# Kernel optimization log

Hardware: AMD Instinct MI355X
Metric: run time of the kernel (lower is better)

The kernel has to match this reference:

```python
import jax, jax.numpy as jnp
import numpy as np

B, N, D = 8, 4096, 256
T = 768          # text_dim
E = 4            # num_experts
K = 2            # top_k
GS = 64          # grid_size = img_size // patch_size
WS = 8           # swin window size
NH = 4           # swin heads
MODES = 16       # fno modes
HID = 4 * D      # mlp hidden


def setup_inputs() -> dict:
    key = jax.random.key(0)
    ks = jax.random.split(key, 40)
    rn = lambda k, s, sc=0.02: jax.random.normal(k, s, jnp.float32) * sc
    return {
        "x": jax.random.normal(ks[0], (B, N, D), jnp.float32),
        "text_embedding": jax.random.normal(ks[1], (B, T), jnp.float32),
        # TopKGating: Linear(D+T->D), ReLU, Linear(D->E)
        "g1_w": rn(ks[2], (D, D + T)), "g1_b": jnp.zeros((D,), jnp.float32),
        "g2_w": rn(ks[3], (E, D)), "g2_b": jnp.zeros((E,), jnp.float32),
        # FNOExpert: SpectralConv2d complex weights (real/imag) + 1x1 conv
        "fno_w1r": rn(ks[4], (D, D, MODES, MODES), 1.0 / D), "fno_w1i": rn(ks[5], (D, D, MODES, MODES), 1.0 / D),
        "fno_w2r": rn(ks[6], (D, D, MODES, MODES), 1.0 / D), "fno_w2i": rn(ks[7], (D, D, MODES, MODES), 1.0 / D),
        "fno_cw": rn(ks[8], (D, D)), "fno_cb": jnp.zeros((D,), jnp.float32),
        # MLPExpert #1
        "m1_w1": rn(ks[9], (HID, D)), "m1_b1": jnp.zeros((HID,), jnp.float32),
        "m1_w2": rn(ks[10], (D, HID)), "m1_b2": jnp.zeros((D,), jnp.float32),
        # WindowAttentionExpert
        "a_ln1w": jnp.ones((D,), jnp.float32), "a_ln1b": jnp.zeros((D,), jnp.float32),
        "a_qkvw": rn(ks[11], (3 * D, D)), "a_qkvb": jnp.zeros((3 * D,), jnp.float32),
        "a_ow": rn(ks[12], (D, D)), "a_ob": jnp.zeros((D,), jnp.float32),
        "a_ln2w": jnp.ones((D,), jnp.float32), "a_ln2b": jnp.zeros((D,), jnp.float32),
        "a_mw1": rn(ks[13], (HID, D)), "a_mb1": jnp.zeros((HID,), jnp.float32),
        "a_mw2": rn(ks[14], (D, HID)), "a_mb2": jnp.zeros((D,), jnp.float32),
        # MLPExpert #2 (extra expert to reach num_experts=4)
        "m2_w1": rn(ks[15], (HID, D)), "m2_b1": jnp.zeros((HID,), jnp.float32),
        "m2_w2": rn(ks[16], (D, HID)), "m2_b2": jnp.zeros((D,), jnp.float32),
    }


def _gelu(v):
    return jax.nn.gelu(v, approximate=False)


def _ln(v, g, b, eps=1e-5):
    m = v.mean(-1, keepdims=True)
    var = ((v - m) ** 2).mean(-1, keepdims=True)
    return (v - m) * jax.lax.rsqrt(var + eps) * g + b


def reference(x, text_embedding, g1_w, g1_b, g2_w, g2_b,
              fno_w1r, fno_w1i, fno_w2r, fno_w2i, fno_cw, fno_cb,
              m1_w1, m1_b1, m1_w2, m1_b2,
              a_ln1w, a_ln1b, a_qkvw, a_qkvb, a_ow, a_ob,
              a_ln2w, a_ln2b, a_mw1, a_mb1, a_mw2, a_mb2,
              m2_w1, m2_b1, m2_w2, m2_b2):
    Bb, Nn, Dd = x.shape

    # ---- TopKGating ----
    feat = jnp.concatenate([x.mean(axis=1), text_embedding], axis=1)   # [B, D+T]
    h = jax.nn.relu(feat @ g1_w.T + g1_b)
    logits = h @ g2_w.T + g2_b                                         # [B, E]
    vals, idx = jax.lax.top_k(logits, K)
    w = jax.nn.softmax(vals, axis=1)                                   # [B, K]
    # per-(sample, expert) combine weight; indices are constants
    combine = (w[..., None] * jax.nn.one_hot(idx, E, dtype=x.dtype)).sum(axis=1)  # [B, E]

    # ---- Expert 0: FNO ----
    def fno(v):
        xg = v.transpose(0, 2, 1).reshape(Bb, Dd, GS, GS)              # [B, D, H, W]
        xft = jnp.fft.rfft2(xg)                                        # [B, D, H, W//2+1]
        w1 = fno_w1r + 1j * fno_w1i
        w2 = fno_w2r + 1j * fno_w2i
        lo = jnp.einsum('bixy,ioxy->boxy', xft[:, :, :MODES, :MODES], w1)
        hi = jnp.einsum('bixy,ioxy->boxy', xft[:, :, -MODES:, :MODES], w2)
        out_ft = jnp.zeros_like(xft)
        out_ft = out_ft.at[:, :, :MODES, :MODES].set(lo)
        out_ft = out_ft.at[:, :, -MODES:, :MODES].set(hi)
        x1 = jnp.fft.irfft2(out_ft, s=(GS, GS))
        x2 = jnp.einsum('bihw,oi->bohw', xg, fno_cw) + fno_cb[None, :, None, None]
        out = _gelu(x1 + x2)
        return out.reshape(Bb, Dd, Nn).transpose(0, 2, 1) + v

    # ---- MLP experts ----
    def mlp(v, w1, b1, w2, b2):
        return _gelu(v @ w1.T + b1) @ w2.T + b2 + v

    # ---- Expert 2: window attention ----
    def win_attn(v):
        xs = _ln(v, a_ln1w, a_ln1b).reshape(Bb, GS, GS, Dd)
        nw = GS // WS
        xw = xs.reshape(Bb, nw, WS, nw, WS, Dd).transpose(0, 1, 3, 2, 4, 5)
        xw = xw.reshape(-1, WS * WS, Dd)                               # [B*nw*nw, L, D]
        qkv = xw @ a_qkvw.T + a_qkvb
        q, k, vv = jnp.split(qkv, 3, axis=-1)
        dh = Dd // NH
        heads = lambda t: t.reshape(-1, WS * WS, NH, dh).transpose(0, 2, 1, 3)
        q, k, vv = heads(q), heads(k), heads(vv)
        attn = jax.nn.softmax(q @ k.transpose(0, 1, 3, 2) / jnp.sqrt(jnp.float32(dh)), axis=-1)
        o = (attn @ vv).transpose(0, 2, 1, 3).reshape(-1, WS * WS, Dd) @ a_ow.T + a_ob
        o = o.reshape(Bb, nw, nw, WS, WS, Dd).transpose(0, 1, 3, 2, 4, 5).reshape(Bb, Nn, Dd)
        v2 = v + o
        return v2 + (_gelu(_ln(v2, a_ln2w, a_ln2b) @ a_mw1.T + a_mb1) @ a_mw2.T + a_mb2)

    outs = [fno(x),
            mlp(x, m1_w1, m1_b1, m1_w2, m1_b2),
            win_attn(x),
            mlp(x, m2_w1, m2_b1, m2_w2, m2_b2)]
    final = sum(combine[:, e, None, None] * outs[e] for e in range(E))
    return final, w
```

## Files before the change

kernel.cpp:

```cpp
#include <hip/hip_runtime.h>
#include <math.h>

#define BB 8
#define NN 4096
#define DDIM 256
#define TT 768
#define BND (BB*NN*DDIM)

typedef unsigned short ushort_t;
typedef short bf16x8 __attribute__((ext_vector_type(8)));
typedef float f32x4 __attribute__((ext_vector_type(4)));

__device__ __forceinline__ float gelu_f(float v){
    float y = 0.7978845608028654f * v * (1.0f + 0.044715f * v * v);
    float ay = fabsf(y);
    float e = __expf(-2.0f * ay);
    float th = 1.0f - 2.0f * e / (1.0f + e);
    th = copysignf(th, y);
    return 0.5f * v * (1.0f + th);
}
__device__ __forceinline__ ushort_t f2bf(float f){
    union { float f; unsigned int u; } v; v.f = f;
    unsigned int u = v.u;
    u += 0x7FFFu + ((u >> 16) & 1u);
    return (ushort_t)(u >> 16);
}
__device__ __forceinline__ float bf2f(ushort_t h){
    union { unsigned int u; float f; } v; v.u = ((unsigned int)h) << 16;
    return v.f;
}
__device__ __forceinline__ float pk_re(unsigned int p){
    union { unsigned int u; float f; } v; v.u = p << 16; return v.f;
}
__device__ __forceinline__ float pk_im(unsigned int p){
    union { unsigned int u; float f; } v; v.u = p & 0xffff0000u; return v.f;
}
#define GLOAD16(gp, lp) __builtin_amdgcn_global_load_lds( \
    (__attribute__((address_space(1))) const void*)(gp),  \
    (__attribute__((address_space(3))) void*)(lp), 16, 0, 0)

__global__ __launch_bounds__(256) void k_xcvt2(const float4* __restrict__ x,
    const float* __restrict__ lng, const float* __restrict__ lnb,
    ushort_t* __restrict__ xbf, ushort_t* __restrict__ xlnbf, float4* __restrict__ outp,
    float* __restrict__ partialA){
    int w = threadIdx.x >> 6, lane = threadIdx.x & 63;
    int row = blockIdx.x*4 + w;
    size_t i4 = (size_t)row*64 + lane;
    float4 v = x[i4];
    outp[i4] = v;
    float vv[4] = {v.x, v.y, v.z, v.w};
    __shared__ float sda[4][256];
    *(float4*)&sda[w][lane*4] = v;
    float s = (vv[0]+vv[1])+(vv[2]+vv[3]);
    float s2 = (vv[0]*vv[0]+vv[1]*vv[1])+(vv[2]*vv[2]+vv[3]*vv[3]);
    for (int off=32; off; off>>=1){ s += __shfl_down(s, off); s2 += __shfl_down(s2, off); }
    float m = __shfl(s, 0) * (1.0f/DDIM);
    float var = __shfl(s2, 0) * (1.0f/DDIM) - m*m;
    float r = rsqrtf(var + 1e-5f);
    int c0 = lane*4;
    #pragma unroll
    for (int u=0;u<4;++u){
        size_t i = i4*4 + u;
        xbf[i] = f2bf(vv[u]);
        xlnbf[i] = f2bf((vv[u]-m)*r*lng[c0+u] + lnb[c0+u]);
    }
    __syncthreads();
    if (w==0){
        float4 a = *(const float4*)&sda[0][lane*4];
        float4 b4 = *(const float4*)&sda[1][lane*4];
        float4 c4 = *(const float4*)&sda[2][lane*4];
        float4 d4 = *(const float4*)&sda[3][lane*4];
        float4 sum = make_float4(a.x+b4.x+c4.x+d4.x, a.y+b4.y+c4.y+d4.y,
                                 a.z+b4.z+c4.z+d4.z, a.w+b4.w+c4.w+d4.w);
        *(float4*)&partialA[(size_t)blockIdx.x*256 + lane*4] = sum;
    }
}

__global__ __launch_bounds__(256) void k_meanB(const float* __restrict__ partialA, float* __restrict__ partialB){
    int seg = blockIdx.x, b = blockIdx.y, t = threadIdx.x;
    const float* p = partialA + ((size_t)(b*1024 + seg*64))*256 + t;
    float s0=0,s1=0,s2=0,s3=0;
    #pragma unroll
    for (int c=0;c<64;c+=4){
        s0 += p[(size_t)c*256];
        s1 += p[(size_t)(c+1)*256];
        s2 += p[(size_t)(c+2)*256];
        s3 += p[(size_t)(c+3)*256];
    }
    partialB[((size_t)b*16 + seg)*256 + t] = (s0+s1)+(s2+s3);
}

__global__ __launch_bounds__(256) void k_gate1(const float* __restrict__ partial, const float* __restrict__ text,
    const float* __restrict__ g1w, const float* __restrict__ g1b, float* __restrict__ hs){
    int d = blockIdx.x, t = threadIdx.x;
    int w = t >> 6, lane = t & 63;
    float xm[BB];
    #pragma unroll
    for (int b=0;b<BB;++b){
        float s = 0.f;
        #pragma unroll
        for (int c=0;c<16;++c) s += partial[((size_t)b*16 + c)*256 + t];
        xm[b] = s * (1.0f/NN);
    }
    const float* wrow = g1w + (size_t)d*(DDIM+TT);
    float w0 = wrow[t], w1 = wrow[256+t], w2 = wrow[512+t], w3 = wrow[768+t];
    float acc[BB];
    #pragma unroll
    for (int b=0;b<BB;++b){
        const float* tx = text + (size_t)b*TT;
        acc[b] = xm[b]*w0 + tx[t]*w1 + tx[256+t]*w2 + tx[512+t]*w3;
    }
    #pragma unroll
    for (int b=0;b<BB;++b)
        for (int off=32; off; off>>=1) acc[b] += __shfl_down(acc[b], off);
    __shared__ float red[BB][4];
    if (lane==0)
        #pragma unroll
        for (int b=0;b<BB;++b) red[b][w] = acc[b];
    __syncthreads();
    if (t < BB){
        float s = red[t][0]+red[t][1]+red[t][2]+red[t][3] + g1b[d];
        hs[t*DDIM + d] = fmaxf(s, 0.0f);
    }
}

__global__ __launch_bounds__(64) void k_gate2(const float* __restrict__ hs,
    const float* __restrict__ g2w, const float* __restrict__ g2b,
    float* __restrict__ combine, float* __restrict__ wout){
    __shared__ float lg[BB][4];
    int t = threadIdx.x;
    if (t < 32){
        int b = t>>2, e = t&3;
        float a = g2b[e];
        const float* w2 = g2w + e*DDIM;
        const float* h = hs + b*DDIM;
        for (int o=0;o<DDIM;o+=4)
            a += h[o]*w2[o] + h[o+1]*w2[o+1] + h[o+2]*w2[o+2] + h[o+3]*w2[o+3];
        lg[b][e] = a;
    }
    __syncthreads();
    if (t < BB){
        int b = t;
        int i1=0; float v1=lg[b][0];
        for (int e=1;e<4;++e){ if (lg[b][e] > v1){ v1=lg[b][e]; i1=e; } }
        int i2=0; float v2=-3.0e38f; bool found=false;
        for (int e=0;e<4;++e){ if (e==i1) continue; if (!found || lg[b][e] > v2){ v2=lg[b][e]; i2=e; found=true; } }
        float e2 = expf(v2 - v1);
        float inv = 1.0f/(1.0f + e2);
        float w0 = inv, w1 = e2*inv;
        float cv[4] = {0.f,0.f,0.f,0.f};
        cv[i1] = w0; cv[i2] = w1;
        for (int e=0;e<4;++e) combine[b*4+e] = cv[e];
        wout[b*2+0] = w0; wout[b*2+1] = w1;
    }
}

__global__ __launch_bounds__(256) void k_cvtw(
    const float* __restrict__ s0, const float* __restrict__ s1, const float* __restrict__ s2,
    const float* __restrict__ s3, const float* __restrict__ s4, const float* __restrict__ s5,
    const float* __restrict__ s6, const float* __restrict__ s7, const float* __restrict__ s8,
    ushort_t* __restrict__ dst){
    const int off[10] = {0,196608,262144,524288,786432,1048576,1310720,1572864,1835008,1900544};
    const float* srcs[9] = {s0,s1,s2,s3,s4,s5,s6,s7,s8};
    int i = (blockIdx.x*256 + threadIdx.x)*8;
    if (i >= 1900544) return;
    int seg = 0;
    #pragma unroll
    for (int k=1;k<9;++k) if (i >= off[k]) seg = k;
    const float* s = srcs[seg] + (i - off[seg]);
    ushort_t* d = dst + i;
    #pragma unroll
    for (int u=0;u<8;++u) d[u] = f2bf(s[u]);
}

__global__ __launch_bounds__(256) void k_v2cvt2(const float4* __restrict__ v2,
    const float* __restrict__ lng, const float* __restrict__ lnb,
    ushort_t* __restrict__ dstbf, const float* __restrict__ combine){
    int w = threadIdx.x >> 6, lane = threadIdx.x & 63;
    int row = blockIdx.x*4 + w;
    if (combine[(row>>12)*4+2]==0.0f) return;
    size_t i4 = (size_t)row*64 + lane;
    float4 v = v2[i4];
    float vv[4] = {v.x, v.y, v.z, v.w};
    float s = (vv[0]+vv[1])+(vv[2]+vv[3]);
    float s2 = (vv[0]*vv[0]+vv[1]*vv[1])+(vv[2]*vv[2]+vv[3]*vv[3]);
    for (int off=32; off; off>>=1){ s += __shfl_down(s, off); s2 += __shfl_down(s2, off); }
    float m = __shfl(s, 0) * (1.0f/DDIM);
    float var = __shfl(s2, 0) * (1.0f/DDIM) - m*m;
    float r = rsqrtf(var + 1e-5f);
    int c0 = lane*4;
    #pragma unroll
    for (int u=0;u<4;++u)
        dstbf[i4*4+u] = f2bf((vv[u]-m)*r*lng[c0+u] + lnb[c0+u]);
}

__global__ __launch_bounds__(256) void k_fft_w2(const ushort_t* __restrict__ xbf, float* __restrict__ F1,
                                                const float* __restrict__ combine){
    int h = blockIdx.x, b = blockIdx.y;
    if (combine[b*4+0]==0.0f) return;
    __shared__ ushort_t img[64*256];
    __shared__ float ct[64], st[64];
    int t = threadIdx.x;
    if (t < 64){ float ang = (float)t * 0.09817477042468103f; ct[t]=cosf(ang); st[t]=sinf(ang); }
    {
        const uint4* src = (const uint4*)(xbf + ((size_t)b*NN + h*64)*DDIM);
        uint4* dst4 = (uint4*)img;
        for (int i=t; i<2048; i+=256) dst4[i] = src[i];
    }
    __syncthreads();
    float re[16], im[16];
    #pragma unroll
    for (int ky=0;ky<16;++ky){ re[ky]=0.f; im[ky]=0.f; }
    for (int w=0; w<64; ++w){
        float v = bf2f(img[w*256 + t]);
        #pragma unroll
        for (int ky=0; ky<16; ++ky){
            int m = (ky*w)&63;
            re[ky] += v*ct[m];
            im[ky] -= v*st[m];
        }
    }
    float2* o = (float2*)(F1 + (((size_t)(b*DDIM + t))*1024 + h*16)*2);
    #pragma unroll
    for (int ky=0;ky<16;++ky) o[ky] = make_float2(re[ky], im[ky]);
}

__global__ __launch_bounds__(256) void k_fft_h(const float* __restrict__ F1,
                                               unsigned int* __restrict__ F2pk,
                                               const float* __restrict__ combine){
    int bd = blockIdx.x; int b = bd>>8;
    if (combine[b*4+0]==0.0f) return;
    __shared__ float f1[2048];
    __shared__ float ct[64], st[64];
    int t = threadIdx.x;
    if (t < 64){ float ang = (float)t * 0.09817477042468103f; ct[t]=cosf(ang); st[t]=sinf(ang); }
    const float* src = F1 + (size_t)bd*2048;
    for (int i=t;i<2048;i+=256) f1[i]=src[i];
    __syncthreads();
    for (int task=t; task<512; task+=256){
        int c = task>>8, kxp = (task>>4)&15, ky = task&15;
        int kx = c ? 48+kxp : kxp;
        float re=0.f, im=0.f;
        #pragma unroll
        for (int h=0;h<64;++h){
            int m = (kx*h)&63;
            float ar = f1[(h*16+ky)*2], ai = f1[(h*16+ky)*2+1];
            re += ar*ct[m] + ai*st[m];
            im += ai*ct[m] - ar*st[m];
        }
        F2pk[(size_t)bd*512 + task] = (((unsigned int)f2bf(im)) << 16) | (unsigned int)f2bf(re);
    }
}

__global__ __launch_bounds__(256, 8) void k_specmul12(const unsigned int* __restrict__ F2pk,
    const float* __restrict__ w1r, const float* __restrict__ w1i,
    const float* __restrict__ w2r, const float* __restrict__ w2i,
    float* __restrict__ Gp, const float* __restrict__ combine){
    bool any=false;
    for (int b=0;b<BB;++b) any = any || (combine[b*4]!=0.0f);
    if (!any) return;
    int t  = threadIdx.x;
    int o0 = blockIdx.x * 2;
    int c  = blockIdx.y;
    int s  = blockIdx.z;
    const float* Wr0 = (c ? w2r : w1r) + ((size_t)(s*32)*DDIM + o0)*256 + t;
    const float* Wi0 = (c ? w2i : w1i) + ((size_t)(s*32)*DDIM + o0)*256 + t;
    const unsigned int* Fp = F2pk + (size_t)(s*32)*512 + c*256 + t;
    float ar[2][BB], ai[2][BB];
    #pragma unroll
    for (int oo=0;oo<2;++oo)
        #pragma unroll
        for (int b=0;b<BB;++b){ ar[oo][b]=0.f; ai[oo][b]=0.f; }
    for (int ii=0; ii<32; ++ii){
        float wr0 = __builtin_nontemporal_load(Wr0);
        float wr1 = __builtin_nontemporal_load(Wr0 + 256);
        float wi0 = __builtin_nontemporal_load(Wi0);
        float wi1 = __builtin_nontemporal_load(Wi0 + 256);
        unsigned int f[BB];
        #pragma unroll
        for (int b=0;b<BB;++b)
            f[b] = Fp[(size_t)b*131072];
        Wr0 += 65536; Wi0 += 65536; Fp += 512;
        #pragma unroll
        for (int b=0;b<BB;++b){
            float fr = pk_re(f[b]);
            float fi = pk_im(f[b]);
            ar[0][b] += fr*wr0 - fi*wi0;
            ai[0][b] += fr*wi0 + fi*wr0;
            ar[1][b] += fr*wr1 - fi*wi1;
            ai[1][b] += fr*wi1 + fi*wr1;
        }
    }
    #pragma unroll
    for (int oo=0;oo<2;++oo)
        for (int b=0;b<BB;++b){
            float* g = Gp + ((((size_t)s*BB + b)*DDIM + o0+oo)*512 + c*256 + t)*2;
            __builtin_nontemporal_store(ar[oo][b], g);
            __builtin_nontemporal_store(ai[oo][b], g+1);
        }
}

__global__ __launch_bounds__(256) void k_ifft_h(const float* __restrict__ Gp, float* __restrict__ Z,
                                                const float* __restrict__ combine){
    int bd = blockIdx.x; int b = bd>>8;
    if (combine[b*4+0]==0.0f) return;
    __shared__ float g[1024];
    __shared__ float ct[64], st[64];
    int t=threadIdx.x;
    if (t < 64){ float ang = (float)t * 0.09817477042468103f; ct[t]=cosf(ang); st[t]=sinf(ang); }
    {
        f32x4 v = (f32x4){0.f,0.f,0.f,0.f};
        #pragma unroll
        for (int s=0;s<8;++s){
            const f32x4* p = (const f32x4*)(Gp + (size_t)s*2097152 + (size_t)bd*1024);
            v += __builtin_nontemporal_load(p + t);
        }
        *(f32x4*)(g + t*4) = v;
    }
    __syncthreads();
    for (int task=t;task<1024;task+=256){
        int h=task>>4, ky=task&15;
        float re=0.f, im=0.f;
        #pragma unroll
        for (int c=0;c<2;++c){
            #pragma unroll
            for (int kxp=0;kxp<16;++kxp){
                int kx = c ? 48+kxp : kxp;
                int m = (kx*h)&63;
                int gi = (c*256 + kxp*16 + ky)*2;
                float gr=g[gi], gim=g[gi+1];
                re += gr*ct[m] - gim*st[m];
                im += gr*st[m] + gim*ct[m];
            }
        }
        float2* o = (float2*)(Z + ((size_t)bd*1024 + task)*2);
        *o = make_float2(re*(1.0f/64.0f), im*(1.0f/64.0f));
    }
}

__global__ __launch_bounds__(256) void k_fno_out(const float* __restrict__ Z, const ushort_t* __restrict__ X2,
    const float* __restrict__ combine, float* __restrict__ out){
    int h = blockIdx.x, b = blockIdx.y;
    float cb = combine[b*4];
    if (cb==0.0f) return;
    __shared__ float ct[64], st[64];
    int t = threadIdx.x;
    if (t < 64){ float ang = (float)t * 0.09817477042468103f; ct[t]=cosf(ang); st[t]=sinf(ang); }
    __syncthreads();
    float zr[16], zi[16];
    const float* zp = Z + (((size_t)(b*DDIM + t)*64 + h)*16)*2;
    #pragma unroll
    for (int ky=0;ky<16;++ky){
        float2 v = *(const float2*)(zp + ky*2);
        zr[ky]=v.x; zi[ky]=v.y;
    }
    for (int w=0;w<64;++w){
        float s = zr[0];
        #pragma unroll
        for (int ky=1;ky<16;++ky){
            int m = (ky*w)&63;
            s += 2.0f*(zr[ky]*ct[m] - zi[ky]*st[m]);
        }
        s *= (1.0f/64.0f);
        size_t idx = ((size_t)b*NN + h*64 + w)*DDIM + t;
        out[idx] += cb * gelu_f(s + bf2f(X2[idx]));
    }
}

template<int EPI>
__global__ __launch_bounds__(256) void k_bgemm(
    const ushort_t* __restrict__ A, const ushort_t* __restrict__ W, const float* __restrict__ bias,
    void* __restrict__ dst, const float* __restrict__ combine, int expert, int K, int N,
    const float* __restrict__ xres, float* __restrict__ out)
{
    int tiles_n = N >> 7;
    int tm = blockIdx.x / tiles_n, tn = blockIdx.x - tm*tiles_n;
    int row0 = tm << 7, col0 = tn << 7;
    float scale = combine[(row0>>12)*4 + expert];
    if (scale == 0.0f) return;
    __shared__ __align__(16) ushort_t As[8192];
    __shared__ __align__(16) ushort_t Bs[8192];
    int t = threadIdx.x;
    int w = t >> 6, lane = t & 63;
    int wr = w >> 1, wc = w & 1;
    int lrow = lane >> 3, lk8 = (lane & 7) * 8;
    f32x4 acc[4][4];
    #pragma unroll
    for (int m=0;m<4;++m)
        #pragma unroll
        for (int n=0;n<4;++n) acc[m][n] = (f32x4){0.f,0.f,0.f,0.f};
    int afr = lane & 15, akr = (lane >> 4) * 8;
    for (int k0=0; k0<K; k0+=64){
        #pragma unroll
        for (int it=0; it<4; ++it){
            int c = it*4 + w;
            const ushort_t* ga = A + (size_t)(row0 + c*8 + lrow)*K + k0 + lk8;
            GLOAD16(ga, As + c*512);
            const ushort_t* gb = W + (size_t)(col0 + c*8 + lrow)*K + k0 + lk8;
            GLOAD16(gb, Bs + c*512);
        }
        __syncthreads();
        #pragma unroll
        for (int kk=0; kk<2; ++kk){
            bf16x8 af[4], bfr[4];
            #pragma unroll
            for (int m=0;m<4;++m)
                af[m] = *(const bf16x8*)(As + (wr*64 + m*16 + afr)*64 + kk*32 + akr);
            #pragma unroll
            for (int n=0;n<4;++n)
                bfr[n] = *(const bf16x8*)(Bs + (wc*64 + n*16 + afr)*64 + kk*32 + akr);
            #pragma unroll
            for (int m=0;m<4;++m)
                #pragma unroll
                for (int n=0;n<4;++n)
                    acc[m][n] = __builtin_amdgcn_mfma_f32_16x16x32_bf16(af[m], bfr[n], acc[m][n], 0, 0, 0);
        }
        __syncthreads();
    }
    int rbase = row0 + wr*64 + (lane>>4)*4;
    int cbase = col0 + wc*64 + (lane&15);
    #pragma unroll
    for (int n=0;n<4;++n){
        int col = cbase + n*16;
        float bcol = bias[col];
        #pragma unroll
        for (int m=0;m<4;++m){
            int r0 = rbase + m*16;
            f32x4 a = acc[m][n];
            #pragma unroll
            for (int j=0;j<4;++j){
                int r = r0 + j;
                float v = a[j] + bcol;
                if (EPI==0)      ((ushort_t*)dst)[(size_t)r*N + col] = f2bf(v);
                else if (EPI==1) ((ushort_t*)dst)[(size_t)r*N + col] = f2bf(gelu_f(v));
                else if (EPI==2) out[(size_t)r*DDIM + col] += scale * v;
                else if (EPI==3){
                    ((float*)dst)[(size_t)r*DDIM + col] = xres[(size_t)r*DDIM + col] + v;
                    out[(size_t)r*DDIM + col] += scale * v;
                }
            }
        }
    }
}

__global__ __launch_bounds__(256) void k_attn(const ushort_t* __restrict__ QKV, ushort_t* __restrict__ O,
                                              const float* __restrict__ combine){
    int wh = blockIdx.x;
    int w = wh>>2, head = wh&3;
    int b = w>>6;
    if (combine[b*4+2]==0.0f) return;
    int i1 = (w>>3)&7, i2 = w&7;
    __shared__ float A1[64][64];
    __shared__ float kk[64][65];
    __shared__ float S[64][65];
    int t = threadIdx.x;
    for (int idx=t; idx<4096; idx+=256){
        int l = idx>>6, dc = idx&63;
        int n = b*NN + (i1*8 + (l>>3))*64 + i2*8 + (l&7);
        const ushort_t* qrow = QKV + (size_t)n*768;
        A1[l][dc] = bf2f(qrow[head*64+dc]);
        kk[l][dc] = bf2f(qrow[256+head*64+dc]);
    }
    __syncthreads();
    for (int idx=t; idx<4096; idx+=256){
        int i=idx>>6, j=idx&63;
        float s=0.f;
        #pragma unroll 8
        for (int dc=0;dc<64;++dc) s += A1[i][dc]*kk[j][dc];
        S[i][j] = s * 0.125f;
    }
    __syncthreads();
    for (int idx=t; idx<4096; idx+=256){
        int l = idx>>6, dc = idx&63;
        int n = b*NN + (i1*8 + (l>>3))*64 + i2*8 + (l&7);
        A1[l][dc] = bf2f(QKV[(size_t)n*768 + 512 + head*64 + dc]);
    }
    __syncthreads();
    if (t < 64){
        float mx = -3.0e38f;
        for (int j=0;j<64;++j) mx = fmaxf(mx, S[t][j]);
        float sum=0.f;
        for (int j=0;j<64;++j){ float e = expf(S[t][j]-mx); S[t][j]=e; sum+=e; }
        float inv = 1.0f/sum;
        for (int j=0;j<64;++j) S[t][j] *= inv;
    }
    __syncthreads();
    for (int idx=t; idx<4096; idx+=256){
        int i=idx>>6, dc=idx&63;
        float s=0.f;
        #pragma unroll 8
        for (int j=0;j<64;++j) s += S[i][j]*A1[j][dc];
        int n = b*NN + (i1*8 + (i>>3))*64 + i2*8 + (i&7);
        O[(size_t)n*DDIM + head*64 + dc] = f2bf(s);
    }
}

extern "C" void kernel_launch(void* const* d_in, const int* in_sizes, int n_in,
                              void* d_out, int out_size, void* d_ws, size_t ws_size,
                              hipStream_t stream) {
    (void)in_sizes; (void)n_in; (void)out_size; (void)ws_size;
    const float* x      = (const float*)d_in[0];
    const float* text   = (const float*)d_in[1];
    const float* g1_w   = (const float*)d_in[2];
    const float* g1_b   = (const float*)d_in[3];
    const float* g2_w   = (const float*)d_in[4];
    const float* g2_b   = (const float*)d_in[5];
    const float* w1r    = (const float*)d_in[6];
    const float* w1i    = (const float*)d_in[7];
    const float* w2r    = (const float*)d_in[8];
    const float* w2i    = (const float*)d_in[9];
    const float* fno_cw = (const float*)d_in[10];
    const float* fno_cb = (const float*)d_in[11];
    const float* m1_w1  = (const float*)d_in[12];
    const float* m1_b1  = (const float*)d_in[13];
    const float* m1_w2  = (const float*)d_in[14];
    const float* m1_b2  = (const float*)d_in[15];
    const float* a_ln1w = (const float*)d_in[16];
    const float* a_ln1b = (const float*)d_in[17];
    const float* a_qkvw = (const float*)d_in[18];
    const float* a_qkvb = (const float*)d_in[19];
    const float* a_ow   = (const float*)d_in[20];
    const float* a_ob   = (const float*)d_in[21];
    const float* a_ln2w = (const float*)d_in[22];
    const float* a_ln2b = (const float*)d_in[23];
    const float* a_mw1  = (const float*)d_in[24];
    const float* a_mb1  = (const float*)d_in[25];
    const float* a_mw2  = (const float*)d_in[26];
    const float* a_mb2  = (const float*)d_in[27];
    const float* m2_w1  = (const float*)d_in[28];
    const float* m2_b1  = (const float*)d_in[29];
    const float* m2_w2  = (const float*)d_in[30];
    const float* m2_b2  = (const float*)d_in[31];

    float* out  = (float*)d_out;
    float* wout = out + (size_t)BND;

    float* wsf     = (float*)d_ws;
    float* hs      = wsf;
    float* combine = wsf + 2048;
    ushort_t* wbf  = (ushort_t*)(wsf + 69632);
    float* partialB = wsf + 1019904;
    ushort_t* x_bf   = (ushort_t*)(wsf + 1118208);
    ushort_t* xln_bf = (ushort_t*)(wsf + 5312512);
    float* R1 = wsf + 9506816;
    float* partialA = R1;
    float* Gp  = R1;
    float* F1  = R1 + 8388608;
    float* Z   = R1 + 16777216;
    ushort_t* X2_bf = (ushort_t*)(R1 + 20971520);
    unsigned int* F2pk = (unsigned int*)(R1 + 29360128);
    ushort_t* QKV_bf  = (ushort_t*)R1;
    ushort_t* O_bf    = (ushort_t*)(R1 + 12582912);
    float*    V2      = R1 + 16777216;
    ushort_t* v2ln_bf = (ushort_t*)(R1 + 25165824);
    ushort_t* H_bf = (ushort_t*)R1;

    ushort_t* qkvw_bf = wbf + 0;
    ushort_t* ow_bf   = wbf + 196608;
    ushort_t* mw1_bf  = wbf + 262144;
    ushort_t* mw2_bf  = wbf + 524288;
    ushort_t* m1w1_bf = wbf + 786432;
    ushort_t* m1w2_bf = wbf + 1048576;
    ushort_t* m2w1_bf = wbf + 1310720;
    ushort_t* m2w2_bf = wbf + 1572864;
    ushort_t* cw_bf   = wbf + 1835008;

    k_xcvt2<<<8192, 256, 0, stream>>>((const float4*)x, a_ln1w, a_ln1b, x_bf, xln_bf, (float4*)out, partialA);
    k_meanB<<<dim3(16,BB), 256, 0, stream>>>(partialA, partialB);
    k_gate1<<<256, 256, 0, stream>>>(partialB, text, g1_w, g1_b, hs);
    k_gate2<<<1, 64, 0, stream>>>(hs, g2_w, g2_b, combine, wout);
    k_cvtw<<<928, 256, 0, stream>>>(a_qkvw, a_ow, a_mw1, a_mw2, m1_w1, m1_w2, m2_w1, m2_w2, fno_cw, wbf);

    k_fft_w2<<<dim3(64,BB), 256, 0, stream>>>(x_bf, F1, combine);
    k_fft_h<<<2048, 256, 0, stream>>>(F1, F2pk, combine);
    k_specmul12<<<dim3(128,2,8), 256, 0, stream>>>(F2pk, w1r, w1i, w2r, w2i, Gp, combine);
    k_ifft_h<<<2048, 256, 0, stream>>>(Gp, Z, combine);
    k_bgemm<0><<<512, 256, 0, stream>>>(x_bf, cw_bf, fno_cb, X2_bf, combine, 0, 256, 256, nullptr, nullptr);
    k_fno_out<<<dim3(64,8), 256, 0, stream>>>(Z, X2_bf, combine, out);

    k_bgemm<1><<<2048, 256, 0, stream>>>(x_bf, m1w1_bf, m1_b1, H_bf, combine, 1, 256, 1024, nullptr, nullptr);
    k_bgemm<2><<<512, 256, 0, stream>>>(H_bf, m1w2_bf, m1_b2, nullptr, combine, 1, 1024, 256, nullptr, out);

    k_bgemm<0><<<1536, 256, 0, stream>>>(xln_bf, qkvw_bf, a_qkvb, QKV_bf, combine, 2, 256, 768, nullptr, nullptr);
    k_attn<<<2048, 256, 0, stream>>>(QKV_bf, O_bf, combine);
    k_bgemm<3><<<512, 256, 0, stream>>>(O_bf, ow_bf, a_ob, V2, combine, 2, 256, 256, x, out);
    k_v2cvt2<<<8192, 256, 0, stream>>>((const float4*)V2, a_ln2w, a_ln2b, v2ln_bf, combine);
    k_bgemm<1><<<2048, 256, 0, stream>>>(v2ln_bf, mw1_bf, a_mb1, H_bf, combine, 2, 256, 1024, nullptr, nullptr);
    k_bgemm<2><<<512, 256, 0, stream>>>(H_bf, mw2_bf, a_mb2, nullptr, combine, 2, 1024, 256, nullptr, out);

    k_bgemm<1><<<2048, 256, 0, stream>>>(x_bf, m2w1_bf, m2_b1, H_bf, combine, 3, 256, 1024, nullptr, nullptr);
    k_bgemm<2><<<512, 256, 0, stream>>>(H_bf, m2w2_bf, m2_b2, nullptr, combine, 3, 1024, 256, nullptr, out);
}
```

Before: 528.7 us.

## Pack spectral partials to bf16, register-block attention, add nontemporal loads

The spectral multiply now writes its per-split partial sums as packed bf16 complex pairs instead of fp32, which halves the intermediate traffic that the inverse FFT reads back. Window attention switches to 16-byte vectorized QKV loads and O stores, computes 8 outputs per thread with register accumulation, and uses the fast exp intrinsic. Several streaming loads (input x, Z, X2) are marked nontemporal. Rounding the partial sums to bf16 before the 8-way reduction adds precision loss.

```diff
diff --git a/kernel.cpp b/kernel.cpp
--- a/kernel.cpp
+++ b/kernel.cpp
@@ -10,6 +10,7 @@
 typedef unsigned short ushort_t;
 typedef short bf16x8 __attribute__((ext_vector_type(8)));
 typedef float f32x4 __attribute__((ext_vector_type(4)));
+typedef unsigned int u32x2 __attribute__((ext_vector_type(2)));
 
 __device__ __forceinline__ float gelu_f(float v){
     float y = 0.7978845608028654f * v * (1.0f + 0.044715f * v * v);
@@ -39,18 +40,18 @@
     (__attribute__((address_space(1))) const void*)(gp),  \
     (__attribute__((address_space(3))) void*)(lp), 16, 0, 0)
 
-__global__ __launch_bounds__(256) void k_xcvt2(const float4* __restrict__ x,
+__global__ __launch_bounds__(256) void k_xcvt2(const float* __restrict__ x,
     const float* __restrict__ lng, const float* __restrict__ lnb,
-    ushort_t* __restrict__ xbf, ushort_t* __restrict__ xlnbf, float4* __restrict__ outp,
+    ushort_t* __restrict__ xbf, ushort_t* __restrict__ xlnbf, float* __restrict__ outp,
     float* __restrict__ partialA){
     int w = threadIdx.x >> 6, lane = threadIdx.x & 63;
     int row = blockIdx.x*4 + w;
     size_t i4 = (size_t)row*64 + lane;
-    float4 v = x[i4];
-    outp[i4] = v;
-    float vv[4] = {v.x, v.y, v.z, v.w};
+    f32x4 v = __builtin_nontemporal_load((const f32x4*)x + i4);
+    *((f32x4*)outp + i4) = v;
+    float vv[4] = {v[0], v[1], v[2], v[3]};
     __shared__ float sda[4][256];
-    *(float4*)&sda[w][lane*4] = v;
+    *(f32x4*)&sda[w][lane*4] = v;
     float s = (vv[0]+vv[1])+(vv[2]+vv[3]);
     float s2 = (vv[0]*vv[0]+vv[1]*vv[1])+(vv[2]*vv[2]+vv[3]*vv[3]);
     for (int off=32; off; off>>=1){ s += __shfl_down(s, off); s2 += __shfl_down(s2, off); }
@@ -66,13 +67,12 @@
     }
     __syncthreads();
     if (w==0){
-        float4 a = *(const float4*)&sda[0][lane*4];
-        float4 b4 = *(const float4*)&sda[1][lane*4];
-        float4 c4 = *(const float4*)&sda[2][lane*4];
-        float4 d4 = *(const float4*)&sda[3][lane*4];
-        float4 sum = make_float4(a.x+b4.x+c4.x+d4.x, a.y+b4.y+c4.y+d4.y,
-                                 a.z+b4.z+c4.z+d4.z, a.w+b4.w+c4.w+d4.w);
-        *(float4*)&partialA[(size_t)blockIdx.x*256 + lane*4] = sum;
+        f32x4 a = *(const f32x4*)&sda[0][lane*4];
+        f32x4 b4 = *(const f32x4*)&sda[1][lane*4];
+        f32x4 c4 = *(const f32x4*)&sda[2][lane*4];
+        f32x4 d4 = *(const f32x4*)&sda[3][lane*4];
+        f32x4 sum = a + b4 + c4 + d4;
+        *(f32x4*)&partialA[(size_t)blockIdx.x*256 + lane*4] = sum;
     }
 }
 
@@ -173,15 +173,15 @@
     for (int u=0;u<8;++u) d[u] = f2bf(s[u]);
 }
 
-__global__ __launch_bounds__(256) void k_v2cvt2(const float4* __restrict__ v2,
+__global__ __launch_bounds__(256) void k_v2cvt2(const float* __restrict__ v2,
     const float* __restrict__ lng, const float* __restrict__ lnb,
     ushort_t* __restrict__ dstbf, const float* __restrict__ combine){
     int w = threadIdx.x >> 6, lane = threadIdx.x & 63;
     int row = blockIdx.x*4 + w;
     if (combine[(row>>12)*4+2]==0.0f) return;
     size_t i4 = (size_t)row*64 + lane;
-    float4 v = v2[i4];
-    float vv[4] = {v.x, v.y, v.z, v.w};
+    f32x4 v = *((const f32x4*)v2 + i4);
+    float vv[4] = {v[0], v[1], v[2], v[3]};
     float s = (vv[0]+vv[1])+(vv[2]+vv[3]);
     float s2 = (vv[0]*vv[0]+vv[1]*vv[1])+(vv[2]*vv[2]+vv[3]*vv[3]);
     for (int off=32; off; off>>=1){ s += __shfl_down(s, off); s2 += __shfl_down(s2, off); }
@@ -252,10 +252,10 @@
     }
 }
 
-__global__ __launch_bounds__(256, 8) void k_specmul12(const unsigned int* __restrict__ F2pk,
+__global__ __launch_bounds__(256, 8) void k_specmul13(const unsigned int* __restrict__ F2pk,
     const float* __restrict__ w1r, const float* __restrict__ w1i,
     const float* __restrict__ w2r, const float* __restrict__ w2i,
-    float* __restrict__ Gp, const float* __restrict__ combine){
+    unsigned int* __restrict__ Gp, const float* __restrict__ combine){
     bool any=false;
     for (int b=0;b<BB;++b) any = any || (combine[b*4]!=0.0f);
     if (!any) return;
@@ -294,15 +294,14 @@
     #pragma unroll
     for (int oo=0;oo<2;++oo)
         for (int b=0;b<BB;++b){
-            float* g = Gp + ((((size_t)s*BB + b)*DDIM + o0+oo)*512 + c*256 + t)*2;
-            __builtin_nontemporal_store(ar[oo][b], g);
-            __builtin_nontemporal_store(ai[oo][b], g+1);
-        }
-}
-
-__global__ __launch_bounds__(256) void k_ifft_h(const float* __restrict__ Gp, float* __restrict__ Z,
+            unsigned int pk = (((unsigned int)f2bf(ai[oo][b])) << 16) | (unsigned int)f2bf(ar[oo][b]);
+            __builtin_nontemporal_store(pk, Gp + (((size_t)(s*BB + b)*DDIM + o0+oo)*512 + c*256 + t));
+        }
+}
+
+__global__ __launch_bounds__(256) void k_ifft_h(const unsigned int* __restrict__ Gp, float* __restrict__ Z,
                                                 const float* __restrict__ combine){
-    int bd = blockIdx.x; int b = bd>>8;
+    int bd = blockIdx.x; int b = bd>>8, d = bd&255;
     if (combine[b*4+0]==0.0f) return;
     __shared__ float g[1024];
     __shared__ float ct[64], st[64];
@@ -312,8 +311,10 @@
         f32x4 v = (f32x4){0.f,0.f,0.f,0.f};
         #pragma unroll
         for (int s=0;s<8;++s){
-            const f32x4* p = (const f32x4*)(Gp + (size_t)s*2097152 + (size_t)bd*1024);
-            v += __builtin_nontemporal_load(p + t);
+            const u32x2* p = (const u32x2*)(Gp + ((size_t)(s*BB + b)*DDIM + d)*512);
+            u32x2 pk = __builtin_nontemporal_load(p + t);
+            v[0] += pk_re(pk[0]); v[1] += pk_im(pk[0]);
+            v[2] += pk_re(pk[1]); v[3] += pk_im(pk[1]);
         }
         *(f32x4*)(g + t*4) = v;
     }
@@ -351,8 +352,9 @@
     const float* zp = Z + (((size_t)(b*DDIM + t)*64 + h)*16)*2;
     #pragma unroll
     for (int ky=0;ky<16;++ky){
-        float2 v = *(const float2*)(zp + ky*2);
-        zr[ky]=v.x; zi[ky]=v.y;
+        float vx = __builtin_nontemporal_load(zp + ky*2);
+        float vy = __builtin_nontemporal_load(zp + ky*2 + 1);
+        zr[ky]=vx; zi[ky]=vy;
     }
     for (int w=0;w<64;++w){
         float s = zr[0];
@@ -363,7 +365,7 @@
         }
         s *= (1.0f/64.0f);
         size_t idx = ((size_t)b*NN + h*64 + w)*DDIM + t;
-        out[idx] += cb * gelu_f(s + bf2f(X2[idx]));
+        out[idx] += cb * gelu_f(s + bf2f(__builtin_nontemporal_load(X2 + idx)));
     }
 }
 
@@ -454,44 +456,65 @@
     __shared__ float kk[64][65];
     __shared__ float S[64][65];
     int t = threadIdx.x;
-    for (int idx=t; idx<4096; idx+=256){
-        int l = idx>>6, dc = idx&63;
+    for (int idx=t; idx<512; idx+=256){
+        int l = idx>>3, dc8 = (idx&7)*8;
         int n = b*NN + (i1*8 + (l>>3))*64 + i2*8 + (l&7);
-        const ushort_t* qrow = QKV + (size_t)n*768;
-        A1[l][dc] = bf2f(qrow[head*64+dc]);
-        kk[l][dc] = bf2f(qrow[256+head*64+dc]);
-    }
-    __syncthreads();
-    for (int idx=t; idx<4096; idx+=256){
-        int i=idx>>6, j=idx&63;
-        float s=0.f;
-        #pragma unroll 8
-        for (int dc=0;dc<64;++dc) s += A1[i][dc]*kk[j][dc];
-        S[i][j] = s * 0.125f;
-    }
-    __syncthreads();
-    for (int idx=t; idx<4096; idx+=256){
-        int l = idx>>6, dc = idx&63;
+        const ushort_t* qrow = QKV + (size_t)n*768 + head*64;
+        uint4 qv = *(const uint4*)(qrow + dc8);
+        uint4 kv = *(const uint4*)(qrow + 256 + dc8);
+        const ushort_t* qp = (const ushort_t*)&qv;
+        const ushort_t* kp = (const ushort_t*)&kv;
+        #pragma unroll
+        for (int u=0;u<8;++u){
+            A1[l][dc8+u] = bf2f(qp[u]);
+            kk[l][dc8+u] = bf2f(kp[u]);
+        }
+    }
+    __syncthreads();
+    for (int idx=t; idx<512; idx+=256){
+        int i = idx>>3, j0 = (idx&7)*8;
+        float s[8] = {0,0,0,0,0,0,0,0};
+        for (int dc=0; dc<64; ++dc){
+            float a = A1[i][dc];
+            #pragma unroll
+            for (int u=0;u<8;++u) s[u] += a * kk[j0+u][dc];
+        }
+        #pragma unroll
+        for (int u=0;u<8;++u) S[i][j0+u] = s[u] * 0.125f;
+    }
+    __syncthreads();
+    for (int idx=t; idx<512; idx+=256){
+        int l = idx>>3, dc8 = (idx&7)*8;
         int n = b*NN + (i1*8 + (l>>3))*64 + i2*8 + (l&7);
-        A1[l][dc] = bf2f(QKV[(size_t)n*768 + 512 + head*64 + dc]);
+        uint4 vv = *(const uint4*)(QKV + (size_t)n*768 + 512 + head*64 + dc8);
+        const ushort_t* vp = (const ushort_t*)&vv;
+        #pragma unroll
+        for (int u=0;u<8;++u) A1[l][dc8+u] = bf2f(vp[u]);
     }
     __syncthreads();
     if (t < 64){
         float mx = -3.0e38f;
         for (int j=0;j<64;++j) mx = fmaxf(mx, S[t][j]);
         float sum=0.f;
-        for (int j=0;j<64;++j){ float e = expf(S[t][j]-mx); S[t][j]=e; sum+=e; }
+        for (int j=0;j<64;++j){ float e = __expf(S[t][j]-mx); S[t][j]=e; sum+=e; }
         float inv = 1.0f/sum;
         for (int j=0;j<64;++j) S[t][j] *= inv;
     }
     __syncthreads();
-    for (int idx=t; idx<4096; idx+=256){
-        int i=idx>>6, dc=idx&63;
-        float s=0.f;
-        #pragma unroll 8
-        for (int j=0;j<64;++j) s += S[i][j]*A1[j][dc];
+    for (int idx=t; idx<512; idx+=256){
+        int i = idx>>3, dc0 = (idx&7)*8;
+        float s[8] = {0,0,0,0,0,0,0,0};
+        for (int j=0;j<64;++j){
+            float p = S[i][j];
+            #pragma unroll
+            for (int u=0;u<8;++u) s[u] += p * A1[j][dc0+u];
+        }
         int n = b*NN + (i1*8 + (i>>3))*64 + i2*8 + (i&7);
-        O[(size_t)n*DDIM + head*64 + dc] = f2bf(s);
+        uint4 ov;
+        ushort_t* op = (ushort_t*)&ov;
+        #pragma unroll
+        for (int u=0;u<8;++u) op[u] = f2bf(s[u]);
+        *(uint4*)(O + (size_t)n*DDIM + head*64 + dc0) = ov;
     }
 }
 
@@ -544,7 +567,7 @@
     ushort_t* xln_bf = (ushort_t*)(wsf + 5312512);
     float* R1 = wsf + 9506816;
     float* partialA = R1;
-    float* Gp  = R1;
+    unsigned int* Gp = (unsigned int*)R1;
     float* F1  = R1 + 8388608;
     float* Z   = R1 + 16777216;
     ushort_t* X2_bf = (ushort_t*)(R1 + 20971520);
@@ -565,7 +588,7 @@
     ushort_t* m2w2_bf = wbf + 1572864;
     ushort_t* cw_bf   = wbf + 1835008;
 
-    k_xcvt2<<<8192, 256, 0, stream>>>((const float4*)x, a_ln1w, a_ln1b, x_bf, xln_bf, (float4*)out, partialA);
+    k_xcvt2<<<8192, 256, 0, stream>>>(x, a_ln1w, a_ln1b, x_bf, xln_bf, out, partialA);
     k_meanB<<<dim3(16,BB), 256, 0, stream>>>(partialA, partialB);
     k_gate1<<<256, 256, 0, stream>>>(partialB, text, g1_w, g1_b, hs);
     k_gate2<<<1, 64, 0, stream>>>(hs, g2_w, g2_b, combine, wout);
@@ -573,7 +596,7 @@
 
     k_fft_w2<<<dim3(64,BB), 256, 0, stream>>>(x_bf, F1, combine);
     k_fft_h<<<2048, 256, 0, stream>>>(F1, F2pk, combine);
-    k_specmul12<<<dim3(128,2,8), 256, 0, stream>>>(F2pk, w1r, w1i, w2r, w2i, Gp, combine);
+    k_specmul13<<<dim3(128,2,8), 256, 0, stream>>>(F2pk, w1r, w1i, w2r, w2i, Gp, combine);
     k_ifft_h<<<2048, 256, 0, stream>>>(Gp, Z, combine);
     k_bgemm<0><<<512, 256, 0, stream>>>(x_bf, cw_bf, fno_cb, X2_bf, combine, 0, 256, 256, nullptr, nullptr);
     k_fno_out<<<dim3(64,8), 256, 0, stream>>>(Z, X2_bf, combine, out);
@@ -584,7 +607,7 @@
     k_bgemm<0><<<1536, 256, 0, stream>>>(xln_bf, qkvw_bf, a_qkvb, QKV_bf, combine, 2, 256, 768, nullptr, nullptr);
     k_attn<<<2048, 256, 0, stream>>>(QKV_bf, O_bf, combine);
     k_bgemm<3><<<512, 256, 0, stream>>>(O_bf, ow_bf, a_ob, V2, combine, 2, 256, 256, x, out);
-    k_v2cvt2<<<8192, 256, 0, stream>>>((const float4*)V2, a_ln2w, a_ln2b, v2ln_bf, combine);
+    k_v2cvt2<<<8192, 256, 0, stream>>>(V2, a_ln2w, a_ln2b, v2ln_bf, combine);
     k_bgemm<1><<<2048, 256, 0, stream>>>(v2ln_bf, mw1_bf, a_mb1, H_bf, combine, 2, 256, 1024, nullptr, nullptr);
     k_bgemm<2><<<512, 256, 0, stream>>>(H_bf, mw2_bf, a_mb2, nullptr, combine, 2, 1024, 256, nullptr, out);
 
```

Result: slower. 602.8 us (+14.0%).
